# Performance work log

Measured on AMD Instinct MI355X. Metric: run time of the kernel, lower is better.

## Reference

```python
import jax, jax.numpy as jnp
import numpy as np

NUM_NODES = 4096
EMBED_DIM = 64
IN_DIM = 256
OUT_DIM = 256
BATCH = 32


def setup_inputs() -> dict:
    key = jax.random.key(0)
    k1, k2, k3 = jax.random.split(key, 3)
    x = jax.random.normal(k1, (BATCH, NUM_NODES, IN_DIM), dtype=jnp.float32)
    node_ids = jnp.arange(NUM_NODES, dtype=jnp.int64)
    emb_table = jax.random.normal(k2, (NUM_NODES, EMBED_DIM), dtype=jnp.float32) * 0.1
    W = jax.random.normal(k3, (IN_DIM, OUT_DIM), dtype=jnp.float32) * (1.0 / np.sqrt(IN_DIM))
    b = jnp.zeros((OUT_DIM,), dtype=jnp.float32)
    return {"x": x, "node_ids": node_ids, "emb_table": emb_table, "W": W, "b": b}


def reference(x, node_ids, emb_table, W, b):
    # Embedding lookup for node ids -> [N, E]
    E = emb_table[node_ids]
    # Adaptive adjacency from embeddings: softmax(relu(E E^T)) over neighbors
    logits = jax.nn.relu(jnp.einsum("ne,me->nm", E, E))  # [N, N]
    adj = jax.nn.softmax(logits, axis=-1)
    # Graph convolution: aggregate neighbor features, then linear + relu
    h = jnp.einsum("nm,bmd->bnd", adj, x)          # [B, N, in_dim]
    out = jax.nn.relu(jnp.einsum("bnd,do->bno", h, W) + b)  # [B, N, out_dim]
    return out
```

## Files before the change

### kernel.cpp

```cpp
#include <hip/hip_runtime.h>

#define NN   4096
#define ED   64
#define DIN  256
#define DOUT 256
#define NB   32

typedef __attribute__((ext_vector_type(8))) short bf16x8;
typedef __attribute__((ext_vector_type(4))) float f32x4;

__device__ __forceinline__ unsigned short f2bf(float f) {
    union { float f; unsigned u; } v; v.f = f;
    unsigned r = v.u + 0x7FFF + ((v.u >> 16) & 1);
    return (unsigned short)(r >> 16);
}
__device__ __forceinline__ float bf2f(unsigned short s) {
    union { unsigned u; float f; } v; v.u = ((unsigned)s) << 16;
    return v.f;
}

#define GLDS16(g, l) __builtin_amdgcn_global_load_lds( \
    (const __attribute__((address_space(1))) void*)(g), \
    (__attribute__((address_space(3))) void*)(l), 16, 0, 0)

__device__ __forceinline__ void fma4(float4& d, float s, const float4& v) {
    d.x = fmaf(s, v.x, d.x);
    d.y = fmaf(s, v.y, d.y);
    d.z = fmaf(s, v.z, d.z);
    d.w = fmaf(s, v.w, d.w);
}

__global__ void k_gather(const float* __restrict__ emb, const int* __restrict__ ids,
                         float* __restrict__ E) {
    int n = blockIdx.x;
    int e = threadIdx.x;
    int id = ids[n];
    id = id < 0 ? 0 : (id >= NN ? NN - 1 : id);
    E[(size_t)n * ED + e] = emb[(size_t)id * ED + e];
}

__global__ __launch_bounds__(256) void k_logits(const float* __restrict__ E,
                                                unsigned short* __restrict__ adjbf) {
    __shared__ __align__(16) float Ea[ED][64 + 4];
    __shared__ __align__(16) float Eb[ED][64 + 4];
    const int tid = threadIdx.x;
    const int ty = tid >> 4, tx = tid & 15;
    const int rb = blockIdx.x, cb = blockIdx.y;

    #pragma unroll
    for (int k = 0; k < 4; ++k) {
        int l = tid + k * 256;
        int row = l >> 4;
        int kq = (l & 15) * 4;
        float4 va = *(const float4*)&E[(size_t)(rb * 64 + row) * ED + kq];
        Ea[kq + 0][row] = va.x; Ea[kq + 1][row] = va.y;
        Ea[kq + 2][row] = va.z; Ea[kq + 3][row] = va.w;
        float4 vb = *(const float4*)&E[(size_t)(cb * 64 + row) * ED + kq];
        Eb[kq + 0][row] = vb.x; Eb[kq + 1][row] = vb.y;
        Eb[kq + 2][row] = vb.z; Eb[kq + 3][row] = vb.w;
    }
    __syncthreads();

    float4 acc[4] = {};
    #pragma unroll
    for (int k = 0; k < ED; ++k) {
        float4 ar = *(const float4*)&Ea[k][ty * 4];
        float4 br = *(const float4*)&Eb[k][tx * 4];
        fma4(acc[0], ar.x, br);
        fma4(acc[1], ar.y, br);
        fma4(acc[2], ar.z, br);
        fma4(acc[3], ar.w, br);
    }

    #pragma unroll
    for (int i = 0; i < 4; ++i) {
        float4 v = acc[i];
        ushort4 s;
        s.x = f2bf(fmaxf(v.x, 0.f)); s.y = f2bf(fmaxf(v.y, 0.f));
        s.z = f2bf(fmaxf(v.z, 0.f)); s.w = f2bf(fmaxf(v.w, 0.f));
        size_t n = (size_t)(rb * 64 + ty * 4 + i);
        *(ushort4*)&adjbf[n * NN + cb * 64 + tx * 4] = s;
    }
}

__global__ __launch_bounds__(256) void k_softmax(unsigned short* __restrict__ adj) {
    __shared__ float red[256];
    const int tid = threadIdx.x;
    const size_t base = (size_t)blockIdx.x * NN + (size_t)tid * 16;

    unsigned short t16[16];
    *(uint4*)&t16[0] = *(const uint4*)&adj[base];
    *(uint4*)&t16[8] = *(const uint4*)&adj[base + 8];
    float v[16];
    float mx = 0.0f;
    #pragma unroll
    for (int j = 0; j < 16; ++j) { v[j] = bf2f(t16[j]); mx = fmaxf(mx, v[j]); }

    red[tid] = mx; __syncthreads();
    for (int off = 128; off > 0; off >>= 1) {
        if (tid < off) red[tid] = fmaxf(red[tid], red[tid + off]);
        __syncthreads();
    }
    mx = red[0];
    __syncthreads();

    float s = 0.f;
    #pragma unroll
    for (int j = 0; j < 16; ++j) { v[j] = expf(v[j] - mx); s += v[j]; }
    red[tid] = s; __syncthreads();
    for (int off = 128; off > 0; off >>= 1) {
        if (tid < off) red[tid] += red[tid + off];
        __syncthreads();
    }
    const float inv = 1.0f / red[0];

    #pragma unroll
    for (int j = 0; j < 16; ++j) t16[j] = f2bf(v[j] * inv);
    *(uint4*)&adj[base]     = *(const uint4*)&t16[0];
    *(uint4*)&adj[base + 8] = *(const uint4*)&t16[8];
}

__global__ void k_wt(const float* __restrict__ W, unsigned short* __restrict__ WT) {
    int m = blockIdx.x;
    int k = threadIdx.x;
    WT[(size_t)m * DIN + k] = f2bf(W[(size_t)k * DOUT + m]);
}

__global__ __launch_bounds__(256) void k_y(const unsigned short* __restrict__ WT,
                                           const float* __restrict__ x,
                                           unsigned short* __restrict__ yT) {
    __shared__ __align__(16) short As[128 * 32];
    __shared__ __align__(16) short Bs[128 * 32];
    const int tid = threadIdx.x;
    const int lane = tid & 63, w = tid >> 6;
    const int wr = (w >> 1) * 64, wc = (w & 1) * 64;
    const int fr = lane & 15, fq = lane >> 4;
    const int m0 = blockIdx.x * 128;
    const int n0 = blockIdx.y * 128;
    const int b  = blockIdx.z;
    const float* xb = x + (size_t)b * NN * DIN;
    const int brow = tid >> 1, bh = (tid & 1) * 16;

    f32x4 acc[4][4];
    #pragma unroll
    for (int i = 0; i < 4; ++i)
        #pragma unroll
        for (int j = 0; j < 4; ++j) acc[i][j] = (f32x4){0.f, 0.f, 0.f, 0.f};

    for (int k0 = 0; k0 < DIN; k0 += 32) {
        __syncthreads();
        #pragma unroll
        for (int i = 0; i < 2; ++i) {
            int idx = (w * 2 + i) * 512 + lane * 8;
            int row = idx >> 5, kk = idx & 31;
            GLDS16(WT + (size_t)(m0 + row) * DIN + k0 + kk, &As[(w * 2 + i) * 512]);
        }
        float fv[16];
        *(float4*)&fv[0]  = *(const float4*)&xb[(size_t)(n0 + brow) * DIN + k0 + bh + 0];
        *(float4*)&fv[4]  = *(const float4*)&xb[(size_t)(n0 + brow) * DIN + k0 + bh + 4];
        *(float4*)&fv[8]  = *(const float4*)&xb[(size_t)(n0 + brow) * DIN + k0 + bh + 8];
        *(float4*)&fv[12] = *(const float4*)&xb[(size_t)(n0 + brow) * DIN + k0 + bh + 12];
        unsigned u[8];
        #pragma unroll
        for (int j = 0; j < 8; ++j)
            u[j] = (unsigned)f2bf(fv[2 * j]) | ((unsigned)f2bf(fv[2 * j + 1]) << 16);
        *(uint4*)&Bs[brow * 32 + bh]     = make_uint4(u[0], u[1], u[2], u[3]);
        *(uint4*)&Bs[brow * 32 + bh + 8] = make_uint4(u[4], u[5], u[6], u[7]);
        __syncthreads();

        bf16x8 a[4], bb[4];
        #pragma unroll
        for (int mi = 0; mi < 4; ++mi)
            a[mi] = *(const bf16x8*)&As[(wr + mi * 16 + fr) * 32 + fq * 8];
        #pragma unroll
        for (int ni = 0; ni < 4; ++ni)
            bb[ni] = *(const bf16x8*)&Bs[(wc + ni * 16 + fr) * 32 + fq * 8];
        #pragma unroll
        for (int mi = 0; mi < 4; ++mi)
            #pragma unroll
            for (int ni = 0; ni < 4; ++ni)
                acc[mi][ni] = __builtin_amdgcn_mfma_f32_16x16x32_bf16(
                    a[mi], bb[ni], acc[mi][ni], 0, 0, 0);
    }

    unsigned short* yb = yT + (size_t)b * DOUT * NN;
    #pragma unroll
    for (int mi = 0; mi < 4; ++mi)
        #pragma unroll
        for (int ni = 0; ni < 4; ++ni)
            #pragma unroll
            for (int r = 0; r < 4; ++r) {
                int row = m0 + wr + mi * 16 + fq * 4 + r;
                int col = n0 + wc + ni * 16 + fr;
                yb[(size_t)row * NN + col] = f2bf(acc[mi][ni][r]);
            }
}

__global__ __launch_bounds__(256, 2) void k_gcn(const unsigned short* __restrict__ adj,
                                                const unsigned short* __restrict__ yT,
                                                const float* __restrict__ bias,
                                                float* __restrict__ out) {
    __shared__ __align__(16) char smem[73728];

    const int tid  = threadIdx.x;
    const int lane = tid & 63, wid = tid >> 6;
    const int fr = lane & 15, fq = lane >> 4;
    const int wr = wid >> 1, wc = wid & 1;
    const int m0 = blockIdx.x * 256;
    const int ny = blockIdx.y;

    const char* Apanel = (const char*)(adj + (size_t)m0 * NN);
    const char* Bpanel = (const char*)(yT + (size_t)ny * 128 * NN);

    #define STAGE_T(ktb, ldsb)                                                   \
        { _Pragma("unroll")                                                      \
          for (int c = 0; c < 4; ++c) {                                          \
              int r = c * 64 + wid * 16 + (lane >> 2);                           \
              int gcol = (((lane & 3) ^ ((r >> 1) & 3)) << 4);                   \
              GLDS16(Apanel + (size_t)r * 8192 + (ktb) + gcol,                   \
                     (ldsb) + c * 4096 + wid * 1024);                            \
          }                                                                      \
          _Pragma("unroll")                                                      \
          for (int c = 0; c < 2; ++c) {                                          \
              int r = c * 64 + wid * 16 + (lane >> 2);                           \
              int gcol = (((lane & 3) ^ ((r >> 1) & 3)) << 4);                   \
              GLDS16(Bpanel + (size_t)r * 8192 + (ktb) + gcol,                   \
                     (ldsb) + 16384 + c * 4096 + wid * 1024);                    \
          } }

    STAGE_T(0,  smem);
    STAGE_T(64, smem + 24576);

    f32x4 acc[8][4];
    #pragma unroll
    for (int i = 0; i < 8; ++i)
        #pragma unroll
        for (int j = 0; j < 4; ++j) acc[i][j] = (f32x4){0.f, 0.f, 0.f, 0.f};

    const int chunksw = (fq ^ ((fr >> 1) & 3)) << 4;
    const int abase = (wr * 128 + fr) * 64 + chunksw;
    const int bbase = 16384 + (wc * 64 + fr) * 64 + chunksw;

    char* cA = smem;
    char* cB = smem + 24576;
    char* cC = smem + 49152;

    for (int t = 0; t < 128; ++t) {
        if (t < 127) { asm volatile("s_waitcnt vmcnt(6)" ::: "memory"); }
        else         { asm volatile("s_waitcnt vmcnt(0)" ::: "memory"); }
        asm volatile("s_barrier" ::: "memory");

        bf16x8 Af[8], Bf[4];
        #pragma unroll
        for (int ni = 0; ni < 4; ++ni) Bf[ni] = *(const bf16x8*)(cA + bbase + ni * 1024);
        #pragma unroll
        for (int mi = 0; mi < 8; ++mi) Af[mi] = *(const bf16x8*)(cA + abase + mi * 1024);

        if (t + 2 < 128) STAGE_T((t + 2) * 64, cC);

        asm volatile("s_waitcnt lgkmcnt(0)" ::: "memory");
        __builtin_amdgcn_sched_barrier(0);
        __builtin_amdgcn_s_setprio(1);
        #pragma unroll
        for (int mi = 0; mi < 8; ++mi)
            #pragma unroll
            for (int ni = 0; ni < 4; ++ni)
                acc[mi][ni] = __builtin_amdgcn_mfma_f32_16x16x32_bf16(
                    Af[mi], Bf[ni], acc[mi][ni], 0, 0, 0);
        __builtin_amdgcn_s_setprio(0);

        char* tmp = cA; cA = cB; cB = cC; cC = tmp;
    }

    const int by = ny >> 1;
    const int dbase = (ny & 1) * 128;
    float bv[4];
    #pragma unroll
    for (int ni = 0; ni < 4; ++ni) bv[ni] = bias[dbase + wc * 64 + ni * 16 + fr];

    #pragma unroll
    for (int am = 0; am < 8; ++am) {
        const int node = m0 + wr * 128 + am * 16 + fq * 4;
        #pragma unroll
        for (int ni = 0; ni < 4; ++ni) {
            const int dcol = dbase + wc * 64 + ni * 16 + fr;
            #pragma unroll
            for (int rr = 0; rr < 4; ++rr) {
                float vv = acc[am][ni][rr] + bv[ni];
                out[((size_t)by * NN + node + rr) * DOUT + dcol] = fmaxf(vv, 0.f);
            }
        }
    }
    #undef STAGE_T
}

extern "C" void kernel_launch(void* const* d_in, const int* in_sizes, int n_in,
                              void* d_out, int out_size, void* d_ws, size_t ws_size,
                              hipStream_t stream) {
    const float* x    = (const float*)d_in[0];
    const int*   ids  = (const int*)d_in[1];
    const float* emb  = (const float*)d_in[2];
    const float* W    = (const float*)d_in[3];
    const float* bias = (const float*)d_in[4];
    float* out = (float*)d_out;

    char* ws = (char*)d_ws;
    unsigned short* adjbf = (unsigned short*)ws;
    float*          E     = (float*)(ws + 33554432);
    unsigned short* WT    = (unsigned short*)(ws + 33554432 + 1048576);
    unsigned short* yT    = (unsigned short*)(ws + 33554432 + 1048576 + 131072);

    k_gather  <<<NN, ED, 0, stream>>>(emb, ids, E);
    k_logits  <<<dim3(NN / 64, NN / 64), 256, 0, stream>>>(E, adjbf);
    k_softmax <<<NN, 256, 0, stream>>>(adjbf);
    k_wt      <<<DOUT, DIN, 0, stream>>>(W, WT);
    k_y       <<<dim3(DOUT / 128, NN / 128, NB), 256, 0, stream>>>(WT, x, yT);
    k_gcn     <<<dim3(16, 64), 256, 0, stream>>>(adjbf, yT, bias, out);
}
```

Baseline: 373.4 us.

## Load B fragments directly from global into registers and simplify A LDS layout

In the GCN aggregation GEMM, the yT (B) operand no longer goes through LDS. Each lane loads its MFMA fragment straight into registers with inline global_load_dwordx4, double-buffered across tiles (even/odd). Only A is staged in LDS, now in a fragment-native contiguous layout with a three-buffer rotation, which shrinks LDS to 48KB and removes the XOR swizzle. The aim is to cut LDS traffic and footprint, but it relies on manual vmcnt accounting around inline-asm loads and on less coalesced per-lane global reads for B.

```diff
diff --git a/kernel.cpp b/kernel.cpp
--- a/kernel.cpp
+++ b/kernel.cpp
@@ -200,7 +200,7 @@
                                                 const unsigned short* __restrict__ yT,
                                                 const float* __restrict__ bias,
                                                 float* __restrict__ out) {
-    __shared__ __align__(16) char smem[73728];
+    __shared__ __align__(16) char smem[49152];
 
     const int tid  = threadIdx.x;
     const int lane = tid & 63, wid = tid >> 6;
@@ -212,24 +212,34 @@
     const char* Apanel = (const char*)(adj + (size_t)m0 * NN);
     const char* Bpanel = (const char*)(yT + (size_t)ny * 128 * NN);
 
-    #define STAGE_T(ktb, ldsb)                                                   \
+    const char* asrc[4];
+    #pragma unroll
+    for (int i = 0; i < 4; ++i)
+        asrc[i] = Apanel + (size_t)((wid * 4 + i) * 16 + fr) * 8192 + fq * 16;
+    const char* bsrc[4];
+    #pragma unroll
+    for (int ni = 0; ni < 4; ++ni)
+        bsrc[ni] = Bpanel + (size_t)(wc * 64 + ni * 16 + fr) * 8192 + fq * 16;
+
+    #define STAGE_A(T, buf)                                                      \
         { _Pragma("unroll")                                                      \
-          for (int c = 0; c < 4; ++c) {                                          \
-              int r = c * 64 + wid * 16 + (lane >> 2);                           \
-              int gcol = (((lane & 3) ^ ((r >> 1) & 3)) << 4);                   \
-              GLDS16(Apanel + (size_t)r * 8192 + (ktb) + gcol,                   \
-                     (ldsb) + c * 4096 + wid * 1024);                            \
-          }                                                                      \
-          _Pragma("unroll")                                                      \
-          for (int c = 0; c < 2; ++c) {                                          \
-              int r = c * 64 + wid * 16 + (lane >> 2);                           \
-              int gcol = (((lane & 3) ^ ((r >> 1) & 3)) << 4);                   \
-              GLDS16(Bpanel + (size_t)r * 8192 + (ktb) + gcol,                   \
-                     (ldsb) + 16384 + c * 4096 + wid * 1024);                    \
-          } }
-
-    STAGE_T(0,  smem);
-    STAGE_T(64, smem + 24576);
+          for (int i = 0; i < 4; ++i)                                            \
+              GLDS16(asrc[i] + (T) * 64, (buf) + (wid * 4 + i) * 1024); }
+    #define LOAD_B(T, dst)                                                       \
+        { _Pragma("unroll")                                                      \
+          for (int ni = 0; ni < 4; ++ni)                                         \
+              asm volatile("global_load_dwordx4 %0, %1, off"                     \
+                           : "=v"(dst[ni]) : "v"(bsrc[ni] + (T) * 64) : "memory"); }
+
+    char* pA = smem;
+    char* pB = smem + 16384;
+    char* pC = smem + 32768;
+
+    bf16x8 Be[4], Bo[4];
+
+    STAGE_A(0, pA);
+    LOAD_B(0, Be);
+    STAGE_A(1, pB);
 
     f32x4 acc[8][4];
     #pragma unroll
@@ -237,39 +247,37 @@
         #pragma unroll
         for (int j = 0; j < 4; ++j) acc[i][j] = (f32x4){0.f, 0.f, 0.f, 0.f};
 
-    const int chunksw = (fq ^ ((fr >> 1) & 3)) << 4;
-    const int abase = (wr * 128 + fr) * 64 + chunksw;
-    const int bbase = 16384 + (wc * 64 + fr) * 64 + chunksw;
-
-    char* cA = smem;
-    char* cB = smem + 24576;
-    char* cC = smem + 49152;
-
-    for (int t = 0; t < 128; ++t) {
-        if (t < 127) { asm volatile("s_waitcnt vmcnt(6)" ::: "memory"); }
-        else         { asm volatile("s_waitcnt vmcnt(0)" ::: "memory"); }
-        asm volatile("s_barrier" ::: "memory");
-
-        bf16x8 Af[8], Bf[4];
-        #pragma unroll
-        for (int ni = 0; ni < 4; ++ni) Bf[ni] = *(const bf16x8*)(cA + bbase + ni * 1024);
-        #pragma unroll
-        for (int mi = 0; mi < 8; ++mi) Af[mi] = *(const bf16x8*)(cA + abase + mi * 1024);
-
-        if (t + 2 < 128) STAGE_T((t + 2) * 64, cC);
-
-        asm volatile("s_waitcnt lgkmcnt(0)" ::: "memory");
-        __builtin_amdgcn_sched_barrier(0);
-        __builtin_amdgcn_s_setprio(1);
-        #pragma unroll
-        for (int mi = 0; mi < 8; ++mi)
-            #pragma unroll
-            for (int ni = 0; ni < 4; ++ni)
-                acc[mi][ni] = __builtin_amdgcn_mfma_f32_16x16x32_bf16(
-                    Af[mi], Bf[ni], acc[mi][ni], 0, 0, 0);
-        __builtin_amdgcn_s_setprio(0);
-
-        char* tmp = cA; cA = cB; cB = cC; cC = tmp;
+    #define TILE(T, Bcur, Bnxt)                                                  \
+      { if ((T) < 127) { asm volatile("s_waitcnt vmcnt(4)" ::: "memory"); }      \
+        else           { asm volatile("s_waitcnt vmcnt(0)" ::: "memory"); }      \
+        __builtin_amdgcn_sched_barrier(0);                                       \
+        asm volatile("s_barrier" ::: "memory");                                  \
+        __builtin_amdgcn_sched_barrier(0);                                       \
+        bf16x8 Af[8];                                                            \
+        _Pragma("unroll")                                                        \
+        for (int mi = 0; mi < 8; ++mi)                                           \
+            Af[mi] = *(const bf16x8*)(pA + (wr * 8 + mi) * 1024 + lane * 16);    \
+        if ((T) + 1 < 128) LOAD_B((T) + 1, Bnxt);                                \
+        if ((T) + 2 < 128) STAGE_A((T) + 2, pC);                                 \
+        __builtin_amdgcn_s_setprio(1);                                           \
+        _Pragma("unroll")                                                        \
+        for (int mi = 0; mi < 4; ++mi)                                           \
+            _Pragma("unroll")                                                    \
+            for (int ni = 0; ni < 4; ++ni)                                       \
+                acc[mi][ni] = __builtin_amdgcn_mfma_f32_16x16x32_bf16(           \
+                    Af[mi], Bcur[ni], acc[mi][ni], 0, 0, 0);                     \
+        _Pragma("unroll")                                                        \
+        for (int mi = 4; mi < 8; ++mi)                                           \
+            _Pragma("unroll")                                                    \
+            for (int ni = 0; ni < 4; ++ni)                                       \
+                acc[mi][ni] = __builtin_amdgcn_mfma_f32_16x16x32_bf16(           \
+                    Af[mi], Bcur[ni], acc[mi][ni], 0, 0, 0);                     \
+        __builtin_amdgcn_s_setprio(0);                                           \
+        { char* t_ = pA; pA = pB; pB = pC; pC = t_; } }
+
+    for (int tp = 0; tp < 64; ++tp) {
+        TILE(tp * 2,     Be, Bo)
+        TILE(tp * 2 + 1, Bo, Be)
     }
 
     const int by = ny >> 1;
@@ -291,7 +299,9 @@
             }
         }
     }
-    #undef STAGE_T
+    #undef STAGE_A
+    #undef LOAD_B
+    #undef TILE
 }
 
 extern "C" void kernel_launch(void* const* d_in, const int* in_sizes, int n_in,
```

Measured after the change: 576.7 us. +54.4%, slower.
